# Kernel optimization log

Hardware: AMD Instinct MI355X
Metric: run time of the kernel (lower is better)

Reference implementation:

```python
import jax, jax.numpy as jnp
import numpy as np

S = 128          # voxel grid resolution per axis
NPB = 50000      # active voxels per batch element
B = 2            # batch size
C_IN = 64
C_OUT = 64
K = 3            # kernel size

# kernel offsets in [-1,0,1]^3, shape [27, 3]
_OFFS = np.stack(np.meshgrid(np.arange(-1, 2), np.arange(-1, 2), np.arange(-1, 2), indexing='ij'), axis=-1).reshape(-1, 3)


def setup_inputs() -> dict:
    rng = np.random.default_rng(0)
    coords_list = []
    for b in range(B):
        lin = rng.choice(S * S * S, size=NPB, replace=False)  # unique voxels
        x = lin // (S * S)
        y = (lin // S) % S
        z = lin % S
        coords_list.append(np.stack([np.full(NPB, b), x, y, z], axis=1))
    coords = jnp.asarray(np.concatenate(coords_list, axis=0), dtype=jnp.int32)  # [N,4]

    key = jax.random.key(0)
    k1, k2, k3 = jax.random.split(key, 3)
    feats = jax.random.normal(k1, (B * NPB, C_IN), dtype=jnp.float32)
    fan1 = C_IN * K ** 3
    fan2 = C_OUT * K ** 3
    W1 = jax.random.normal(k2, (K ** 3, C_IN, C_OUT), dtype=jnp.float32) / np.sqrt(fan1)
    W2 = jax.random.normal(k3, (K ** 3, C_OUT, C_OUT), dtype=jnp.float32) / np.sqrt(fan2)
    return {"feats": feats, "coords": coords, "W1": W1, "W2": W2}


def _encode(coords):
    # linear key: ((b*S + x)*S + y)*S + z ; fits in int32 for S=128, B small
    b, x, y, z = coords[:, 0], coords[:, 1], coords[:, 2], coords[:, 3]
    return ((b * S + x) * S + y) * S + z


def _sparse_conv(feats, coords, W):
    """Stride-1 sparse (submanifold-style) 3D conv: output coords == input coords.
    feats [N,Cin], coords [N,4], W [27,Cin,Cout] -> [N,Cout]."""
    N = feats.shape[0]
    keys = _encode(coords)
    order = jnp.argsort(keys)
    skeys = keys[order]
    offs = jnp.asarray(_OFFS, dtype=jnp.int32)  # [27,3]

    def gather_one(d):
        qxyz = coords[:, 1:4] + d[None, :]
        valid = jnp.all((qxyz >= 0) & (qxyz < S), axis=1)
        qkey = keys + (d[0] * S * S + d[1] * S + d[2])
        idx = jnp.clip(jnp.searchsorted(skeys, qkey), 0, N - 1)
        found = valid & (skeys[idx] == qkey)
        return jnp.where(found[:, None], feats[order[idx]], 0.0)  # [N,Cin]

    gathered = jax.vmap(gather_one)(offs)  # [27, N, Cin]
    return jnp.einsum('onc,ocd->nd', gathered, W)


def reference(feats, coords, W1, W2):
    h = _sparse_conv(feats, coords, W1)
    out = _sparse_conv(h, coords, W2)
    return out
```

## Files before the change

### kernel.cpp

```cpp
#include <hip/hip_runtime.h>
#include <stdint.h>

#define SGRID 128
#define CAP 4096

typedef _Float16 f16;
typedef f16 f16x8 __attribute__((ext_vector_type(8)));
typedef float f32x4 __attribute__((ext_vector_type(4)));

static __device__ __forceinline__ f32x4 mfma16(uint4 a, uint4 b, f32x4 c) {
    union { uint4 u; f16x8 v; } ua, ub;
    ua.u = a; ub.u = b;
    return __builtin_amdgcn_mfma_f32_16x16x32_f16(ua.v, ub.v, c, 0, 0, 0);
}

static __device__ __forceinline__ void split8(const float* v, uint4& hu, uint4& lu) {
    union { f16 h[8]; uint4 u; } hv, lv;
    #pragma unroll
    for (int j = 0; j < 8; ++j) {
        f16 h = (f16)v[j];
        hv.h[j] = h;
        lv.h[j] = (f16)(v[j] - (float)h);
    }
    hu = hv.u; lu = lv.u;
}

static __device__ __forceinline__ void center_body(
    const float* __restrict__ A, const f16* __restrict__ Wp,
    float* __restrict__ O, int N, int gw, int lane)
{
    const int r = lane & 15, lq = lane >> 4;
    const int p0 = gw * 32;

    const uint4* wb = (const uint4*)Wp + 13 * 512 + lane;
    uint4 b[2][4];
    #pragma unroll
    for (int ct = 0; ct < 4; ++ct)
        #pragma unroll
        for (int ks = 0; ks < 2; ++ks)
            b[ks][ct] = wb[(ct * 2 + ks) * 64];

    uint4 ah[2][2], al[2][2];
    #pragma unroll
    for (int rt = 0; rt < 2; ++rt) {
        int row = p0 + rt * 16 + r;
        #pragma unroll
        for (int ks = 0; ks < 2; ++ks) {
            float v[8];
            if (row < N) {
                float4 v0 = *(const float4*)(A + (size_t)row * 64 + ks * 32 + lq * 8);
                float4 v1 = *(const float4*)(A + (size_t)row * 64 + ks * 32 + lq * 8 + 4);
                v[0]=v0.x; v[1]=v0.y; v[2]=v0.z; v[3]=v0.w;
                v[4]=v1.x; v[5]=v1.y; v[6]=v1.z; v[7]=v1.w;
            } else {
                #pragma unroll
                for (int j = 0; j < 8; ++j) v[j] = 0.f;
            }
            split8(v, ah[rt][ks], al[rt][ks]);
        }
    }

    f32x4 acc[2][4];
    #pragma unroll
    for (int i = 0; i < 2; ++i)
        #pragma unroll
        for (int j = 0; j < 4; ++j) acc[i][j] = (f32x4){0.f, 0.f, 0.f, 0.f};

    #pragma unroll
    for (int ks = 0; ks < 2; ++ks)
        #pragma unroll
        for (int rt = 0; rt < 2; ++rt)
            #pragma unroll
            for (int ct = 0; ct < 4; ++ct) {
                acc[rt][ct] = mfma16(ah[rt][ks], b[ks][ct], acc[rt][ct]);
                acc[rt][ct] = mfma16(al[rt][ks], b[ks][ct], acc[rt][ct]);
            }

    #pragma unroll
    for (int rt = 0; rt < 2; ++rt)
        #pragma unroll
        for (int j = 0; j < 4; ++j) {
            int row = p0 + rt * 16 + lq * 4 + j;
            if (row < N) {
                #pragma unroll
                for (int ct = 0; ct < 4; ++ct)
                    O[(size_t)row * 64 + ct * 16 + r] = acc[rt][ct][j];
            }
        }
}

__global__ void clear_meta(uint4* __restrict__ bitmap4, int nwords4, int* __restrict__ cnt) {
    int i = blockIdx.x * 256 + threadIdx.x;
    if (i < nwords4) bitmap4[i] = (uint4){0, 0, 0, 0};
    if (blockIdx.x == 0 && threadIdx.x < 26) cnt[threadIdx.x * 16] = 0;
}

__global__ void __launch_bounds__(256) scatter_prep(
    const int* __restrict__ coords, int* __restrict__ table,
    unsigned* __restrict__ bitmap, int N, int scatB,
    const float* __restrict__ W1, const float* __restrict__ W2,
    f16* __restrict__ Wp1, f16* __restrict__ Wp2)
{
    const int tid = threadIdx.x;
    if (blockIdx.x < scatB) {
        int i = blockIdx.x * 256 + tid;
        if (i < N) {
            int4 c = ((const int4*)coords)[i];
            int key = ((c.x * SGRID + c.y) * SGRID + c.z) * SGRID + c.w;
            table[key] = i;
            atomicOr(&bitmap[key >> 5], 1u << (key & 31));
        }
        return;
    }
    int idx = (blockIdx.x - scatB) * 256 + tid;
    const int half = 27 * 512;
    const float* W = (idx < half) ? W1 : W2;
    f16* Wp = (idx < half) ? Wp1 : Wp2;
    int id = (idx < half) ? idx : idx - half;
    int lane = id & 63;
    int ks = (id >> 6) & 1;
    int ct = (id >> 7) & 3;
    int o  = id >> 9;
    int co  = ct * 16 + (lane & 15);
    int ci0 = ks * 32 + (lane >> 4) * 8;
    union { f16 h[8]; uint4 u; } hv;
    #pragma unroll
    for (int j = 0; j < 8; ++j)
        hv.h[j] = (f16)W[((size_t)o * 64 + ci0 + j) * 64 + co];
    ((uint4*)Wp)[id] = hv.u;
}

__global__ void __launch_bounds__(256) build_center(
    const int* __restrict__ coords, const int* __restrict__ table,
    const unsigned* __restrict__ bitmap,
    int* __restrict__ pin, int* __restrict__ pout, int* __restrict__ cnt,
    int N, int buildB,
    const float* __restrict__ F, const f16* __restrict__ Wp, float* __restrict__ H)
{
    __shared__ unsigned long long sbal[26][4];
    __shared__ int sbase[26];
    const int tid = threadIdx.x;

    if (blockIdx.x >= buildB) {
        int gw = ((blockIdx.x - buildB) * 256 + tid) >> 6;
        if (gw < (N + 31) >> 5)
            center_body(F, Wp, H, N, gw, tid & 63);
        return;
    }

    const int lane = tid & 63;
    const int wave = tid >> 6;
    const int n    = blockIdx.x * 256 + tid;
    const bool valid = n < N;

    int4 c = {0, 0, 0, 0};
    if (valid) c = ((const int4*)coords)[n];
    const int key = ((c.x * SGRID + c.y) * SGRID + c.z) * SGRID + c.w;

    int nb[26];
    #pragma unroll
    for (int slot = 0; slot < 26; ++slot) {
        int o = slot < 13 ? slot : slot + 1;
        int dx = o / 9 - 1, dy = (o / 3) % 3 - 1, dz = o % 3 - 1;
        int qx = c.y + dx, qy = c.z + dy, qz = c.w + dz;
        nb[slot] = -1;
        if (valid && (unsigned)qx < SGRID && (unsigned)qy < SGRID && (unsigned)qz < SGRID) {
            int qkey = key + (dx * SGRID * SGRID + dy * SGRID + dz);
            if ((bitmap[qkey >> 5] >> (qkey & 31)) & 1u)
                nb[slot] = table[qkey];
        }
    }

    #pragma unroll
    for (int slot = 0; slot < 26; ++slot) {
        unsigned long long bal = __ballot(nb[slot] >= 0);
        if (lane == 0) sbal[slot][wave] = bal;
    }
    __syncthreads();

    if (tid < 26) {
        int tot = (int)__popcll(sbal[tid][0]) + (int)__popcll(sbal[tid][1])
                + (int)__popcll(sbal[tid][2]) + (int)__popcll(sbal[tid][3]);
        int base = 0;
        if (tot) base = atomicAdd(&cnt[tid * 16], tot);
        sbase[tid] = base;
    }
    __syncthreads();

    #pragma unroll
    for (int slot = 0; slot < 26; ++slot) {
        if (nb[slot] >= 0) {
            int rank = (int)__popcll(sbal[slot][wave] & ((1ull << lane) - 1ull));
            #pragma unroll
            for (int w = 0; w < 4; ++w)
                if (w < wave) rank += (int)__popcll(sbal[slot][w]);
            int pos = sbase[slot] + rank;
            if (pos < CAP) {
                pin[slot * CAP + pos]  = nb[slot];
                pout[slot * CAP + pos] = n;
            }
        }
    }
}

__global__ void __launch_bounds__(256) conv_center(
    const float* __restrict__ A, const f16* __restrict__ Wp,
    float* __restrict__ O, int N)
{
    int gw = (blockIdx.x * 256 + threadIdx.x) >> 6;
    if (gw < (N + 31) >> 5)
        center_body(A, Wp, O, N, gw, threadIdx.x & 63);
}

__global__ void __launch_bounds__(256) conv_sparse(
    const float* __restrict__ A, const f16* __restrict__ Wp,
    const int* __restrict__ pin, const int* __restrict__ pout,
    const int* __restrict__ cnt, float* __restrict__ O)
{
    int w = (blockIdx.x * 256 + threadIdx.x) >> 6;
    if (w >= 26 * 512) return;
    int slot  = w >> 9;
    int rem   = w & 511;
    int chunk = rem >> 1;
    int ch    = rem & 1;
    int cn = cnt[slot * 16]; if (cn > CAP) cn = CAP;
    int i0 = chunk * 16;
    if (i0 >= cn) return;
    int o = slot < 13 ? slot : slot + 1;
    const int lane = threadIdx.x & 63, r = lane & 15, lq = lane >> 4;

    const uint4* wb = (const uint4*)Wp + (size_t)o * 512 + lane;
    uint4 b[2][2];
    #pragma unroll
    for (int ct = 0; ct < 2; ++ct)
        #pragma unroll
        for (int ks = 0; ks < 2; ++ks)
            b[ct][ks] = wb[((ch * 2 + ct) * 2 + ks) * 64];

    int p = i0 + r;
    int in = (p < cn) ? pin[slot * CAP + p] : -1;
    uint4 ah[2], al[2];
    #pragma unroll
    for (int ks = 0; ks < 2; ++ks) {
        float v[8];
        if (in >= 0) {
            float4 v0 = *(const float4*)(A + (size_t)in * 64 + ks * 32 + lq * 8);
            float4 v1 = *(const float4*)(A + (size_t)in * 64 + ks * 32 + lq * 8 + 4);
            v[0]=v0.x; v[1]=v0.y; v[2]=v0.z; v[3]=v0.w;
            v[4]=v1.x; v[5]=v1.y; v[6]=v1.z; v[7]=v1.w;
        } else {
            #pragma unroll
            for (int j = 0; j < 8; ++j) v[j] = 0.f;
        }
        split8(v, ah[ks], al[ks]);
    }

    f32x4 acc[2];
    acc[0] = (f32x4){0.f, 0.f, 0.f, 0.f};
    acc[1] = (f32x4){0.f, 0.f, 0.f, 0.f};
    #pragma unroll
    for (int ks = 0; ks < 2; ++ks)
        #pragma unroll
        for (int ct = 0; ct < 2; ++ct) {
            acc[ct] = mfma16(ah[ks], b[ct][ks], acc[ct]);
            acc[ct] = mfma16(al[ks], b[ct][ks], acc[ct]);
        }

    #pragma unroll
    for (int j = 0; j < 4; ++j) {
        int pr = i0 + lq * 4 + j;
        if (pr < cn) {
            int oidx = pout[slot * CAP + pr];
            #pragma unroll
            for (int ct = 0; ct < 2; ++ct)
                atomicAdd(&O[(size_t)oidx * 64 + (ch * 2 + ct) * 16 + r], acc[ct][j]);
        }
    }
}

extern "C" void kernel_launch(void* const* d_in, const int* in_sizes, int n_in,
                              void* d_out, int out_size, void* d_ws, size_t ws_size,
                              hipStream_t stream) {
    const float* feats  = (const float*)d_in[0];
    const int*   coords = (const int*)d_in[1];
    const float* W1     = (const float*)d_in[2];
    const float* W2     = (const float*)d_in[3];
    float* out = (float*)d_out;

    const int N = in_sizes[0] / 64;
    const size_t nvox = 2ull * SGRID * SGRID * SGRID;

    char* p = (char*)d_ws;
    int*      table  = (int*)p;      p += nvox * 4;
    unsigned* bitmap = (unsigned*)p; p += (nvox / 32) * 4;
    int*      cnt    = (int*)p;      p += 26 * 16 * 4;
    int*      pin    = (int*)p;      p += 26ull * CAP * 4;
    int*      pout   = (int*)p;      p += 26ull * CAP * 4;
    float*    H      = (float*)p;    p += (size_t)N * 64 * 4;
    f16*      Wp1    = (f16*)p;      p += 27ull * 4096 * 2;
    f16*      Wp2    = (f16*)p;      p += 27ull * 4096 * 2;

    const int bm4     = (int)(nvox / 32 / 4);
    const int scatB   = (N + 255) / 256;
    const int buildB  = scatB;
    const int ngroups = (N + 31) / 32;
    const int centerB = (ngroups + 3) / 4;
    const int sparseB = 26 * 512 / 4;

    clear_meta<<<(bm4 + 255) / 256, 256, 0, stream>>>((uint4*)bitmap, bm4, cnt);
    scatter_prep<<<scatB + 108, 256, 0, stream>>>(coords, table, bitmap, N, scatB,
                                                  W1, W2, Wp1, Wp2);
    build_center<<<buildB + centerB, 256, 0, stream>>>(coords, table, bitmap,
                                                       pin, pout, cnt, N, buildB,
                                                       feats, Wp1, H);
    conv_sparse<<<sparseB, 256, 0, stream>>>(feats, Wp1, pin, pout, cnt, H);
    conv_center<<<centerB, 256, 0, stream>>>(H, Wp2, out, N);
    conv_sparse<<<sparseB, 256, 0, stream>>>(H, Wp2, pin, pout, cnt, out);
}
```

Measured before the change: 95.77 us.

## Build neighbor lists from column bitmap words and split center conv launch

The neighbor build now reads two bitmap words per (dx,dy) column and extracts a 3-bit z-window, producing a 27-bit occupancy mask instead of 26 separate bitmap probes. Table lookups happen only for occupied neighbors, and per-wave prefix bases are precomputed in shared memory. The fused build+center launch is split so the center conv runs as its own kernel, clear_meta becomes a grid-stride loop with 128 blocks, and the bitmap gets a padding word for the over-read. This cuts scattered memory traffic in the build step, but adds an extra launch and drops the overlap the fused kernel had.

New measurement: 100.9 us. 1.05x slower.

```diff
diff --git a/kernel.cpp b/kernel.cpp
--- a/kernel.cpp
+++ b/kernel.cpp
@@ -7,6 +7,7 @@
 typedef _Float16 f16;
 typedef f16 f16x8 __attribute__((ext_vector_type(8)));
 typedef float f32x4 __attribute__((ext_vector_type(4)));
+typedef unsigned long long u64;
 
 static __device__ __forceinline__ f32x4 mfma16(uint4 a, uint4 b, f32x4 c) {
     union { uint4 u; f16x8 v; } ua, ub;
@@ -90,8 +91,9 @@
 }
 
 __global__ void clear_meta(uint4* __restrict__ bitmap4, int nwords4, int* __restrict__ cnt) {
-    int i = blockIdx.x * 256 + threadIdx.x;
-    if (i < nwords4) bitmap4[i] = (uint4){0, 0, 0, 0};
+    const int stride = gridDim.x * 256;
+    for (int i = blockIdx.x * 256 + threadIdx.x; i < nwords4; i += stride)
+        bitmap4[i] = (uint4){0, 0, 0, 0};
     if (blockIdx.x == 0 && threadIdx.x < 26) cnt[threadIdx.x * 16] = 0;
 }
 
@@ -130,75 +132,82 @@
     ((uint4*)Wp)[id] = hv.u;
 }
 
-__global__ void __launch_bounds__(256) build_center(
+__global__ void __launch_bounds__(256) build(
     const int* __restrict__ coords, const int* __restrict__ table,
     const unsigned* __restrict__ bitmap,
-    int* __restrict__ pin, int* __restrict__ pout, int* __restrict__ cnt,
-    int N, int buildB,
-    const float* __restrict__ F, const f16* __restrict__ Wp, float* __restrict__ H)
-{
-    __shared__ unsigned long long sbal[26][4];
-    __shared__ int sbase[26];
-    const int tid = threadIdx.x;
-
-    if (blockIdx.x >= buildB) {
-        int gw = ((blockIdx.x - buildB) * 256 + tid) >> 6;
-        if (gw < (N + 31) >> 5)
-            center_body(F, Wp, H, N, gw, tid & 63);
-        return;
-    }
-
-    const int lane = tid & 63;
-    const int wave = tid >> 6;
-    const int n    = blockIdx.x * 256 + tid;
+    int* __restrict__ pin, int* __restrict__ pout, int* __restrict__ cnt, int N)
+{
+    __shared__ u64 sbal[26][4];
+    __shared__ int sbase4[26][4];
+
+    const int tid = threadIdx.x, lane = tid & 63, wave = tid >> 6;
+    const int n = blockIdx.x * 256 + tid;
     const bool valid = n < N;
 
     int4 c = {0, 0, 0, 0};
     if (valid) c = ((const int4*)coords)[n];
-    const int key = ((c.x * SGRID + c.y) * SGRID + c.z) * SGRID + c.w;
-
-    int nb[26];
-    #pragma unroll
-    for (int slot = 0; slot < 26; ++slot) {
-        int o = slot < 13 ? slot : slot + 1;
-        int dx = o / 9 - 1, dy = (o / 3) % 3 - 1, dz = o % 3 - 1;
-        int qx = c.y + dx, qy = c.z + dy, qz = c.w + dz;
-        nb[slot] = -1;
-        if (valid && (unsigned)qx < SGRID && (unsigned)qy < SGRID && (unsigned)qz < SGRID) {
-            int qkey = key + (dx * SGRID * SGRID + dy * SGRID + dz);
-            if ((bitmap[qkey >> 5] >> (qkey & 31)) & 1u)
-                nb[slot] = table[qkey];
-        }
-    }
-
-    #pragma unroll
-    for (int slot = 0; slot < 26; ++slot) {
-        unsigned long long bal = __ballot(nb[slot] >= 0);
-        if (lane == 0) sbal[slot][wave] = bal;
+    const int z  = c.w;
+    const int zb = (z == 0) ? 0 : z - 1;
+    const int wofs = zb >> 5, sh = zb & 31;
+
+    unsigned omask = 0;
+    #pragma unroll
+    for (int cidx = 0; cidx < 9; ++cidx) {
+        int dx = cidx / 3 - 1, dy = cidx % 3 - 1;
+        int qx = c.y + dx, qy = c.z + dy;
+        bool colok = valid && ((unsigned)qx < SGRID) && ((unsigned)qy < SGRID);
+        int colbase = ((c.x * SGRID + qx) * SGRID + qy) << 2;
+        int wi = colok ? (colbase + wofs) : 0;
+        unsigned w0 = bitmap[wi];
+        unsigned w1 = bitmap[wi + 1];
+        u64 w = (u64)w0 | ((u64)w1 << 32);
+        unsigned t = (unsigned)(w >> sh) & 7u;
+        if (z == 0)         t = (t << 1) & 6u;
+        if (z == SGRID - 1) t &= 3u;
+        t = colok ? t : 0u;
+        omask |= t << (cidx * 3);
+    }
+    omask &= ~(1u << 13);
+
+    #pragma unroll
+    for (int s = 0; s < 26; ++s) {
+        int o = s < 13 ? s : s + 1;
+        u64 bal = __ballot((omask >> o) & 1u);
+        if (lane == 0) sbal[s][wave] = bal;
     }
     __syncthreads();
 
     if (tid < 26) {
-        int tot = (int)__popcll(sbal[tid][0]) + (int)__popcll(sbal[tid][1])
-                + (int)__popcll(sbal[tid][2]) + (int)__popcll(sbal[tid][3]);
-        int base = 0;
-        if (tot) base = atomicAdd(&cnt[tid * 16], tot);
-        sbase[tid] = base;
+        int c0 = (int)__popcll(sbal[tid][0]);
+        int c1 = (int)__popcll(sbal[tid][1]);
+        int c2 = (int)__popcll(sbal[tid][2]);
+        int c3 = (int)__popcll(sbal[tid][3]);
+        int tot = c0 + c1 + c2 + c3;
+        int base = tot ? atomicAdd(&cnt[tid * 16], tot) : 0;
+        sbase4[tid][0] = base;
+        sbase4[tid][1] = base + c0;
+        sbase4[tid][2] = base + c0 + c1;
+        sbase4[tid][3] = base + c0 + c1 + c2;
     }
     __syncthreads();
 
-    #pragma unroll
-    for (int slot = 0; slot < 26; ++slot) {
-        if (nb[slot] >= 0) {
-            int rank = (int)__popcll(sbal[slot][wave] & ((1ull << lane) - 1ull));
-            #pragma unroll
-            for (int w = 0; w < 4; ++w)
-                if (w < wave) rank += (int)__popcll(sbal[slot][w]);
-            int pos = sbase[slot] + rank;
-            if (pos < CAP) {
-                pin[slot * CAP + pos]  = nb[slot];
-                pout[slot * CAP + pos] = n;
-            }
+    const int key = ((c.x * SGRID + c.y) * SGRID + c.z) * SGRID + z;
+    const u64 ltmask = (1ull << lane) - 1ull;
+    unsigned m = omask;
+    while (m) {
+        int o = __ffs(m) - 1;
+        m &= m - 1;
+        int s = o - (o > 13 ? 1 : 0);
+        int dx = o / 9 - 1;
+        int r9 = o - (dx + 1) * 9;
+        int dy = r9 / 3 - 1;
+        int dz = r9 - (dy + 1) * 3 - 1;
+        int qkey = key + dx * SGRID * SGRID + dy * SGRID + dz;
+        int v = table[qkey];
+        int pos = sbase4[s][wave] + (int)__popcll(sbal[s][wave] & ltmask);
+        if (pos < CAP) {
+            pin[s * CAP + pos]  = v;
+            pout[s * CAP + pos] = n;
         }
     }
 }
@@ -293,6 +302,7 @@
     char* p = (char*)d_ws;
     int*      table  = (int*)p;      p += nvox * 4;
     unsigned* bitmap = (unsigned*)p; p += (nvox / 32) * 4;
+    p += 16;
     int*      cnt    = (int*)p;      p += 26 * 16 * 4;
     int*      pin    = (int*)p;      p += 26ull * CAP * 4;
     int*      pout   = (int*)p;      p += 26ull * CAP * 4;
@@ -300,19 +310,17 @@
     f16*      Wp1    = (f16*)p;      p += 27ull * 4096 * 2;
     f16*      Wp2    = (f16*)p;      p += 27ull * 4096 * 2;
 
-    const int bm4     = (int)(nvox / 32 / 4);
+    const int bm4     = (int)(nvox / 32 / 4) + 1;
     const int scatB   = (N + 255) / 256;
-    const int buildB  = scatB;
     const int ngroups = (N + 31) / 32;
     const int centerB = (ngroups + 3) / 4;
     const int sparseB = 26 * 512 / 4;
 
-    clear_meta<<<(bm4 + 255) / 256, 256, 0, stream>>>((uint4*)bitmap, bm4, cnt);
+    clear_meta<<<128, 256, 0, stream>>>((uint4*)bitmap, bm4, cnt);
     scatter_prep<<<scatB + 108, 256, 0, stream>>>(coords, table, bitmap, N, scatB,
                                                   W1, W2, Wp1, Wp2);
-    build_center<<<buildB + centerB, 256, 0, stream>>>(coords, table, bitmap,
-                                                       pin, pout, cnt, N, buildB,
-                                                       feats, Wp1, H);
+    build<<<scatB, 256, 0, stream>>>(coords, table, bitmap, pin, pout, cnt, N);
+    conv_center<<<centerB, 256, 0, stream>>>(feats, Wp1, H, N);
     conv_sparse<<<sparseB, 256, 0, stream>>>(feats, Wp1, pin, pout, cnt, H);
     conv_center<<<centerB, 256, 0, stream>>>(H, Wp2, out, N);
     conv_sparse<<<sparseB, 256, 0, stream>>>(H, Wp2, pin, pout, cnt, out);
```
